# Performance work log

Measured on AMD Instinct MI355X. Metric: run time of the kernel, lower is better.

The kernel has to match this reference:

```python
import jax, jax.numpy as jnp
import numpy as np

N = 100000       # nodes
E = 1600000      # directed edges
D_IN = 64        # input feature dim
D_H = 128        # per-head hidden (num_hidden=256 // 2 heads)
D_OUT = 128      # per-head output (out_dim=256 // 2 heads)
DIR_SEQS = ("OI", "UU")  # per-head direction sequences (already length num_layers=2)
H = len(DIR_SEQS)


def _glorot(key, shape):
    # xavier_uniform with relu gain, matching reset_parameters
    gain = np.sqrt(2.0)
    fan_out, fan_in = shape[-2], shape[-1]
    limit = gain * np.sqrt(6.0 / (fan_in + fan_out))
    return jax.random.uniform(key, shape, jnp.float32, -limit, limit)


def setup_inputs() -> dict:
    key = jax.random.key(0)
    ks = jax.random.split(key, 10)
    x = jax.random.normal(ks[0], (N, D_IN), jnp.float32)
    src = jax.random.randint(ks[1], (E,), 0, N, dtype=jnp.int32)
    dst = jax.random.randint(ks[2], (E,), 0, N, dtype=jnp.int32)
    # stacked per-head params: layer0 (D_IN -> D_H), layer1 (D_H -> D_OUT)
    Wn0 = _glorot(ks[3], (H, D_H, D_IN))
    Ws0 = _glorot(ks[4], (H, D_H, D_IN))
    b0 = jnp.zeros((H, D_H), jnp.float32)
    Wn1 = _glorot(ks[5], (H, D_OUT, D_H))
    Ws1 = _glorot(ks[6], (H, D_OUT, D_H))
    b1 = jnp.zeros((H, D_OUT), jnp.float32)
    return {"x": x, "src": src, "dst": dst,
            "Wn0": Wn0, "Ws0": Ws0, "b0": b0,
            "Wn1": Wn1, "Ws1": Ws1, "b1": b1}


def reference(x, src, dst, Wn0, Ws0, b0, Wn1, Ws1, b1):
    def seg_mean(feat, s, d):
        # DGL mean reduce: zero for nodes with no in-edges
        summ = jax.ops.segment_sum(feat[s], d, num_segments=N)          # [N, F]
        deg = jax.ops.segment_sum(jnp.ones((s.shape[0], 1), feat.dtype), d, num_segments=N)
        return jnp.where(deg > 0, summ / jnp.maximum(deg, 1.0), 0.0)

    def edges_for(c):
        if c == 'O':   # original graph: messages src -> dst
            return src, dst
        if c == 'I':   # reversed graph
            return dst, src
        # 'U': undirected = both directions
        return jnp.concatenate([src, dst]), jnp.concatenate([dst, src])

    def sage_layer(h, s, d, Wn, Ws, b, act):
        in_f, out_f = Wn.shape[1], Wn.shape[0]
        if in_f > out_f:  # lin_before_mp
            h_neigh = seg_mean(h @ Wn.T, s, d)
        else:
            h_neigh = seg_mean(h, s, d) @ Wn.T
        r = h @ Ws.T + b + h_neigh
        return jax.nn.relu(r) if act else r

    outs = []
    for hi, dseq in enumerate(DIR_SEQS):
        h = x
        layers = [(Wn0[hi], Ws0[hi], b0[hi], True),    # hidden layer: relu, no norm
                  (Wn1[hi], Ws1[hi], b1[hi], False)]   # last layer: encoding=False -> no act
        for (Wn, Ws, b, act), c in zip(layers, dseq):
            s, d = edges_for(c)
            h = sage_layer(h, s, d, Wn, Ws, b, act)
        outs.append(h)
    return jnp.concatenate(outs, axis=-1)  # [N, H*D_OUT]
```

## Files before the change

kernel.cpp:

```cpp
#include <hip/hip_runtime.h>
#include <hip/hip_fp8.h>


typedef unsigned short u16;
typedef unsigned int u32;
typedef unsigned char u8;
typedef __bf16 bf16x8 __attribute__((ext_vector_type(8)));
typedef float f32x4 __attribute__((ext_vector_type(4)));

__device__ __forceinline__ u32 f2bf(float f) {
    u32 u = __float_as_uint(f);
    return (u + 0x7fffu + ((u >> 16) & 1u)) >> 16;
}
__device__ __forceinline__ float bf_lo(u32 v) { return __uint_as_float(v << 16); }
__device__ __forceinline__ float bf_hi(u32 v) { return __uint_as_float(v & 0xffff0000u); }
__device__ __forceinline__ u8 f2q(float f) {
    __hip_fp8_e4m3 t(f);
    return *(u8*)&t;
}
__device__ __forceinline__ u32 sprd(u32 v) {
    return __builtin_amdgcn_perm(0u, v, 0x04010400u);
}
__device__ __forceinline__ void acc4(float4& s, u32 v) {
    s.x += __builtin_amdgcn_cvt_f32_fp8(v, 0);
    s.y += __builtin_amdgcn_cvt_f32_fp8(v, 1);
    s.z += __builtin_amdgcn_cvt_f32_fp8(v, 2);
    s.w += __builtin_amdgcn_cvt_f32_fp8(v, 3);
}

__global__ void k_prep(const float* __restrict__ x, u16* __restrict__ xb,
                       u8* __restrict__ xq, int n4, int* __restrict__ cntzero,
                       int* __restrict__ maxzero,
                       const float* __restrict__ Ws0, const float* __restrict__ Wn0,
                       const float* __restrict__ Ws1, const float* __restrict__ Wn1,
                       u16* __restrict__ Wsb0, u16* __restrict__ Wnb0,
                       u16* __restrict__ Wsb1, u16* __restrict__ Wnb1) {
    int i = blockIdx.x * blockDim.x + threadIdx.x;
    if (i < 1024) cntzero[i] = 0;
    if (i < 256) maxzero[i] = 0;
    if (i < n4) {
        float4 v = *(const float4*)&x[(size_t)i * 4];
        u32 p0 = f2bf(v.x) | (f2bf(v.y) << 16);
        u32 p1 = f2bf(v.z) | (f2bf(v.w) << 16);
        *(uint2*)&xb[(size_t)i * 4] = make_uint2(p0, p1);
        u32 q = (u32)f2q(v.x) | ((u32)f2q(v.y) << 8) |
                ((u32)f2q(v.z) << 16) | ((u32)f2q(v.w) << 24);
        *(u32*)&xq[(size_t)i * 4] = q;
        return;
    }
    int t = i - n4;
    if (t < 16384) Wsb0[t] = (u16)f2bf(Ws0[t]);
    else if (t < 32768) Wnb0[t - 16384] = (u16)f2bf(Wn0[t - 16384]);
    else if (t < 65536) Wsb1[t - 32768] = (u16)f2bf(Ws1[t - 32768]);
    else if (t < 98304) Wnb1[t - 65536] = (u16)f2bf(Wn1[t - 65536]);
}


__global__ void __launch_bounds__(256) k_bincnt(
        const int* __restrict__ src, const int* __restrict__ dst,
        int* cntD, int* cntS, int E, int NB) {
    __shared__ int hD[512], hS[512];
    const int tid = threadIdx.x;
    for (int i = tid; i < NB; i += 256) { hD[i] = 0; hS[i] = 0; }
    __syncthreads();
    const int base = (blockIdx.x * 256 + tid) * 8;
#pragma unroll
    for (int i = 0; i < 8; i++) {
        if (base + i < E) {
            atomicAdd(&hD[dst[base + i] >> 8], 1);
            atomicAdd(&hS[src[base + i] >> 8], 1);
        }
    }
    __syncthreads();
    for (int i = tid; i < NB; i += 256) {
        if (hD[i]) atomicAdd(&cntD[i], hD[i]);
        if (hS[i]) atomicAdd(&cntS[i], hS[i]);
    }
}

__global__ void __launch_bounds__(512) k_binscan(
        const int* __restrict__ cntD, const int* __restrict__ cntS,
        int* bbaseD, int* bbaseS, int* curD, int* curS,
        int* off_in, int* off_out, int NB, int N, int E) {
    __shared__ int ts[512];
    const int tid = threadIdx.x;
    int v = (tid < NB) ? cntD[tid] : 0;
    ts[tid] = v;
    __syncthreads();
    for (int ofs = 1; ofs < 512; ofs <<= 1) {
        int t = (tid >= ofs) ? ts[tid - ofs] : 0;
        __syncthreads();
        ts[tid] += t;
        __syncthreads();
    }
    int ex = ts[tid] - v;
    if (tid < NB) { bbaseD[tid] = ex; curD[tid] = ex; }
    if (tid == NB - 1) bbaseD[NB] = ex + v;
    __syncthreads();
    v = (tid < NB) ? cntS[tid] : 0;
    ts[tid] = v;
    __syncthreads();
    for (int ofs = 1; ofs < 512; ofs <<= 1) {
        int t = (tid >= ofs) ? ts[tid - ofs] : 0;
        __syncthreads();
        ts[tid] += t;
        __syncthreads();
    }
    ex = ts[tid] - v;
    if (tid < NB) { bbaseS[tid] = ex; curS[tid] = ex; }
    if (tid == NB - 1) bbaseS[NB] = ex + v;
    if (tid == 0) { off_in[N] = E; off_out[N] = E; }
}

__global__ void __launch_bounds__(256) k_binscatter(
        const int* __restrict__ src, const int* __restrict__ dst,
        int* curD, int* curS, u32* __restrict__ pairsD, u32* __restrict__ pairsS,
        int E, int NB) {
    __shared__ int hD[512], hS[512], bD[512], bS[512];
    const int tid = threadIdx.x;
    for (int i = tid; i < NB; i += 256) { hD[i] = 0; hS[i] = 0; }
    __syncthreads();
    const int base = (blockIdx.x * 256 + tid) * 8;
    int sv[8], dv[8], rD[8], rS[8];
#pragma unroll
    for (int i = 0; i < 8; i++) {
        if (base + i < E) {
            sv[i] = src[base + i];
            dv[i] = dst[base + i];
            rD[i] = atomicAdd(&hD[dv[i] >> 8], 1);
            rS[i] = atomicAdd(&hS[sv[i] >> 8], 1);
        }
    }
    __syncthreads();
    for (int i = tid; i < NB; i += 256) {
        bD[i] = hD[i] ? atomicAdd(&curD[i], hD[i]) : 0;
        bS[i] = hS[i] ? atomicAdd(&curS[i], hS[i]) : 0;
    }
    __syncthreads();
#pragma unroll
    for (int i = 0; i < 8; i++) {
        if (base + i < E) {
            pairsD[bD[dv[i] >> 8] + rD[i]] = ((u32)(dv[i] & 255) << 24) | (u32)sv[i];
            pairsS[bS[sv[i] >> 8] + rS[i]] = ((u32)(sv[i] & 255) << 24) | (u32)dv[i];
        }
    }
}

__global__ void __launch_bounds__(256) k_bucket_csr(
        const u32* __restrict__ pairsD, const u32* __restrict__ pairsS,
        const int* __restrict__ bbaseD, const int* __restrict__ bbaseS,
        int* __restrict__ off_in, int* __restrict__ adj_in,
        int* __restrict__ off_out, int* __restrict__ adj_out, int N) {
    __shared__ int cnt[256], cur[256], ts[256];
    const int b = blockIdx.x >> 1;
    const int arr = blockIdx.x & 1;
    const u32* pairs = arr ? pairsS : pairsD;
    const int* bbase = arr ? bbaseS : bbaseD;
    int* off = arr ? off_out : off_in;
    int* adj = arr ? adj_out : adj_in;
    const int e0 = bbase[b], e1 = bbase[b + 1];
    const int tid = threadIdx.x;
    cnt[tid] = 0;
    __syncthreads();
    for (int e = e0 + tid; e < e1; e += 256) atomicAdd(&cnt[pairs[e] >> 24], 1);
    __syncthreads();
    int v = cnt[tid];
    ts[tid] = v;
    __syncthreads();
    for (int ofs = 1; ofs < 256; ofs <<= 1) {
        int t = (tid >= ofs) ? ts[tid - ofs] : 0;
        __syncthreads();
        ts[tid] += t;
        __syncthreads();
    }
    const int ex = ts[tid] - v;
    const int n = b * 256 + tid;
    if (n < N) off[n] = e0 + ex;
    cur[tid] = e0 + ex;
    __syncthreads();
    for (int e = e0 + tid; e < e1; e += 256) {
        u32 p = pairs[e];
        int w = atomicAdd(&cur[p >> 24], 1);
        adj[w] = (int)(p & 0xFFFFFFu);
    }
}

__global__ void __launch_bounds__(256) k_agg_l0_q(
        const u8* __restrict__ xq,
        const int* __restrict__ off_in, const int* __restrict__ adj_in,
        const int* __restrict__ off_out, const int* __restrict__ adj_out,
        u16* __restrict__ agg0b, u16* __restrict__ aggUb, int n) {
    const int node = blockIdx.x * 4 + (threadIdx.x >> 6);
    const int lane = threadIdx.x & 63;
    if (node >= n) return;
    const int g = lane >> 4;
    const int p = (lane & 15) * 4;
    const int a0 = off_in[node], a1 = off_in[node + 1];
    const int b0 = off_out[node], b1 = off_out[node + 1];
    float4 si = {0.f, 0.f, 0.f, 0.f}, so = {0.f, 0.f, 0.f, 0.f};
    int j = a0;
    for (; j + 15 < a1; j += 16) {
        int i0 = adj_in[j + g], i1 = adj_in[j + 4 + g];
        int i2 = adj_in[j + 8 + g], i3 = adj_in[j + 12 + g];
        u32 v0 = *(const u32*)&xq[(size_t)i0 * 64 + p];
        u32 v1 = *(const u32*)&xq[(size_t)i1 * 64 + p];
        u32 v2 = *(const u32*)&xq[(size_t)i2 * 64 + p];
        u32 v3 = *(const u32*)&xq[(size_t)i3 * 64 + p];
        acc4(si, v0); acc4(si, v1); acc4(si, v2); acc4(si, v3);
    }
    for (; j + 3 < a1; j += 4) {
        int i0 = adj_in[j + g];
        u32 v0 = *(const u32*)&xq[(size_t)i0 * 64 + p];
        acc4(si, v0);
    }
    if (j < a1 && g < a1 - j) {
        int i0 = adj_in[j + g];
        u32 v0 = *(const u32*)&xq[(size_t)i0 * 64 + p];
        acc4(si, v0);
    }
    j = b0;
    for (; j + 15 < b1; j += 16) {
        int i0 = adj_out[j + g], i1 = adj_out[j + 4 + g];
        int i2 = adj_out[j + 8 + g], i3 = adj_out[j + 12 + g];
        u32 v0 = *(const u32*)&xq[(size_t)i0 * 64 + p];
        u32 v1 = *(const u32*)&xq[(size_t)i1 * 64 + p];
        u32 v2 = *(const u32*)&xq[(size_t)i2 * 64 + p];
        u32 v3 = *(const u32*)&xq[(size_t)i3 * 64 + p];
        acc4(so, v0); acc4(so, v1); acc4(so, v2); acc4(so, v3);
    }
    for (; j + 3 < b1; j += 4) {
        int i0 = adj_out[j + g];
        u32 v0 = *(const u32*)&xq[(size_t)i0 * 64 + p];
        acc4(so, v0);
    }
    if (j < b1 && g < b1 - j) {
        int i0 = adj_out[j + g];
        u32 v0 = *(const u32*)&xq[(size_t)i0 * 64 + p];
        acc4(so, v0);
    }
#pragma unroll
    for (int ofs = 16; ofs < 64; ofs <<= 1) {
        si.x += __shfl_xor(si.x, ofs);
        si.y += __shfl_xor(si.y, ofs);
        si.z += __shfl_xor(si.z, ofs);
        si.w += __shfl_xor(si.w, ofs);
        so.x += __shfl_xor(so.x, ofs);
        so.y += __shfl_xor(so.y, ofs);
        so.z += __shfl_xor(so.z, ofs);
        so.w += __shfl_xor(so.w, ofs);
    }
    if (g == 0) {
        const int din = a1 - a0, dout = b1 - b0;
        const int du = din + dout;
        const float fi = din ? 1.f / (float)din : 0.f;
        const float fu = du ? 1.f / (float)du : 0.f;
        uint2 q0, qU;
        q0.x = f2bf(si.x * fi) | (f2bf(si.y * fi) << 16);
        q0.y = f2bf(si.z * fi) | (f2bf(si.w * fi) << 16);
        qU.x = f2bf((si.x + so.x) * fu) | (f2bf((si.y + so.y) * fu) << 16);
        qU.y = f2bf((si.z + so.z) * fu) | (f2bf((si.w + so.w) * fu) << 16);
        *(uint2*)&agg0b[(size_t)node * 64 + p] = q0;
        *(uint2*)&aggUb[(size_t)node * 64 + p] = qU;
    }
}

__global__ void __launch_bounds__(256) k_quant(
        const u16* __restrict__ h1b, const u16* __restrict__ u1b,
        const float* __restrict__ maxH, const float* __restrict__ maxU,
        u8* __restrict__ ob, int N) {
    int i = blockIdx.x * blockDim.x + threadIdx.x;
    const int total = N * 16;
    if (i >= 2 * total) return;
    const int head = (i >= total) ? 1 : 0;
    int t = i - head * total;
    const int row = t >> 4, seg = t & 15;
    const u16* src = head ? u1b : h1b;
    const float* mx = head ? maxU : maxH;
    uint4 v = *(const uint4*)&src[(size_t)row * 128 + seg * 8];
    float4 m0 = *(const float4*)&mx[seg * 8];
    float4 m1 = *(const float4*)&mx[seg * 8 + 4];
    float rs0 = m0.x > 0.f ? 255.f / m0.x : 0.f;
    float rs1 = m0.y > 0.f ? 255.f / m0.y : 0.f;
    float rs2 = m0.z > 0.f ? 255.f / m0.z : 0.f;
    float rs3 = m0.w > 0.f ? 255.f / m0.w : 0.f;
    float rs4 = m1.x > 0.f ? 255.f / m1.x : 0.f;
    float rs5 = m1.y > 0.f ? 255.f / m1.y : 0.f;
    float rs6 = m1.z > 0.f ? 255.f / m1.z : 0.f;
    float rs7 = m1.w > 0.f ? 255.f / m1.w : 0.f;
    u32 q0 = (u32)fminf(rintf(bf_lo(v.x) * rs0), 255.f);
    u32 q1 = (u32)fminf(rintf(bf_hi(v.x) * rs1), 255.f);
    u32 q2 = (u32)fminf(rintf(bf_lo(v.y) * rs2), 255.f);
    u32 q3 = (u32)fminf(rintf(bf_hi(v.y) * rs3), 255.f);
    u32 q4 = (u32)fminf(rintf(bf_lo(v.z) * rs4), 255.f);
    u32 q5 = (u32)fminf(rintf(bf_hi(v.z) * rs5), 255.f);
    u32 q6 = (u32)fminf(rintf(bf_lo(v.w) * rs6), 255.f);
    u32 q7 = (u32)fminf(rintf(bf_hi(v.w) * rs7), 255.f);
    uint2 p;
    p.x = q0 | (q1 << 8) | (q2 << 16) | (q3 << 24);
    p.y = q4 | (q5 << 8) | (q6 << 16) | (q7 << 24);
    *(uint2*)(ob + ((size_t)row << 10) + head * 128 + seg * 8) = p;
}

__global__ void __launch_bounds__(256) k_agg_l1_f(
        const u8* __restrict__ ob,
        const int* __restrict__ off_in, const int* __restrict__ adj_in,
        const int* __restrict__ off_out, const int* __restrict__ adj_out,
        const float* __restrict__ maxH, const float* __restrict__ maxU,
        u16* __restrict__ aggH, int n) {
    const int node = blockIdx.x * 4 + (threadIdx.x >> 6);
    const int lane = threadIdx.x & 63;
    if (node >= n) return;
    const int a0 = off_out[node], a1 = off_out[node + 1];
    const int b0 = off_in[node], b1 = off_in[node + 1];
    u32 sH0 = 0, sH1 = 0, sU0 = 0, sU1 = 0;
    const int lo2 = lane * 2;
    int j = a0;
    for (; j + 7 < a1; j += 8) {
        size_t p0 = ((size_t)adj_out[j] << 10) + lo2;
        size_t p1 = ((size_t)adj_out[j + 1] << 10) + lo2;
        size_t p2 = ((size_t)adj_out[j + 2] << 10) + lo2;
        size_t p3 = ((size_t)adj_out[j + 3] << 10) + lo2;
        size_t p4 = ((size_t)adj_out[j + 4] << 10) + lo2;
        size_t p5 = ((size_t)adj_out[j + 5] << 10) + lo2;
        size_t p6 = ((size_t)adj_out[j + 6] << 10) + lo2;
        size_t p7 = ((size_t)adj_out[j + 7] << 10) + lo2;
        u32 h0 = *(const u16*)(ob + p0), u0 = *(const u16*)(ob + p0 + 128);
        u32 h1 = *(const u16*)(ob + p1), u1 = *(const u16*)(ob + p1 + 128);
        u32 h2 = *(const u16*)(ob + p2), u2 = *(const u16*)(ob + p2 + 128);
        u32 h3 = *(const u16*)(ob + p3), u3 = *(const u16*)(ob + p3 + 128);
        u32 h4 = *(const u16*)(ob + p4), u4 = *(const u16*)(ob + p4 + 128);
        u32 h5 = *(const u16*)(ob + p5), u5 = *(const u16*)(ob + p5 + 128);
        u32 h6 = *(const u16*)(ob + p6), u6 = *(const u16*)(ob + p6 + 128);
        u32 h7 = *(const u16*)(ob + p7), u7 = *(const u16*)(ob + p7 + 128);
        u32 aH = ((sprd(h0) + sprd(h1)) + (sprd(h2) + sprd(h3))) +
                 ((sprd(h4) + sprd(h5)) + (sprd(h6) + sprd(h7)));
        u32 aU = ((sprd(u0) + sprd(u1)) + (sprd(u2) + sprd(u3))) +
                 ((sprd(u4) + sprd(u5)) + (sprd(u6) + sprd(u7)));
        sH0 += aH & 0xFFFFu; sH1 += aH >> 16;
        sU0 += aU & 0xFFFFu; sU1 += aU >> 16;
    }
    for (; j < a1; j++) {
        size_t p = ((size_t)adj_out[j] << 10) + lo2;
        u32 h = *(const u16*)(ob + p), u = *(const u16*)(ob + p + 128);
        sH0 += h & 255; sH1 += h >> 8;
        sU0 += u & 255; sU1 += u >> 8;
    }
    j = b0;
    for (; j + 7 < b1; j += 8) {
        size_t p0 = ((size_t)adj_in[j] << 10) + lo2 + 128;
        size_t p1 = ((size_t)adj_in[j + 1] << 10) + lo2 + 128;
        size_t p2 = ((size_t)adj_in[j + 2] << 10) + lo2 + 128;
        size_t p3 = ((size_t)adj_in[j + 3] << 10) + lo2 + 128;
        size_t p4 = ((size_t)adj_in[j + 4] << 10) + lo2 + 128;
        size_t p5 = ((size_t)adj_in[j + 5] << 10) + lo2 + 128;
        size_t p6 = ((size_t)adj_in[j + 6] << 10) + lo2 + 128;
        size_t p7 = ((size_t)adj_in[j + 7] << 10) + lo2 + 128;
        u32 u0 = *(const u16*)(ob + p0), u1 = *(const u16*)(ob + p1);
        u32 u2 = *(const u16*)(ob + p2), u3 = *(const u16*)(ob + p3);
        u32 u4 = *(const u16*)(ob + p4), u5 = *(const u16*)(ob + p5);
        u32 u6 = *(const u16*)(ob + p6), u7 = *(const u16*)(ob + p7);
        u32 aU = ((sprd(u0) + sprd(u1)) + (sprd(u2) + sprd(u3))) +
                 ((sprd(u4) + sprd(u5)) + (sprd(u6) + sprd(u7)));
        sU0 += aU & 0xFFFFu; sU1 += aU >> 16;
    }
    for (; j < b1; j++) {
        size_t p = ((size_t)adj_in[j] << 10) + lo2 + 128;
        u32 u = *(const u16*)(ob + p);
        sU0 += u & 255; sU1 += u >> 8;
    }
    const int degO = a1 - a0;
    const int degU = degO + (b1 - b0);
    const float invO = degO ? 1.f / (float)degO : 0.f;
    const float invU = degU ? 1.f / (float)degU : 0.f;
    float2 mh = *(const float2*)&maxH[lo2];
    float2 mu = *(const float2*)&maxU[lo2];
    const float c = 1.f / 255.f;
    u32 pH = f2bf((float)sH0 * mh.x * c * invO) |
             (f2bf((float)sH1 * mh.y * c * invO) << 16);
    u32 pU = f2bf((float)sU0 * mu.x * c * invU) |
             (f2bf((float)sU1 * mu.y * c * invU) << 16);
    *(u32*)&aggH[(size_t)node * 128 + lo2] = pH;
    *(u32*)((u8*)ob + ((size_t)node << 10) + 768 + lane * 4) = pU;
}

template <int KC, int OUT_BF16>
__device__ __forceinline__ void gemm_tile(
        const u16* __restrict__ A, int lda,
        const u16* __restrict__ B, int ldb,
        const u16* __restrict__ W1, const u16* __restrict__ W2,
        u8* lds1, u8* lds2, int* lmax,
        const float* __restrict__ bias,
        float* __restrict__ OutF, int ldo, u16* __restrict__ OutB,
        int* __restrict__ colmax, int n, int r0, int nthreads) {
    constexpr int K = KC * 32;
    constexpr int RS = K * 2;
    constexpr int WB = 128 * RS;
    const int tid = threadIdx.x;
    const int lane = tid & 63;

    for (int i = tid * 16; i < WB; i += nthreads * 16) {
        const int row = i / RS;
        const int swz = i ^ ((row & 7) << 4);
        *(uint4*)(lds1 + swz) = *(const uint4*)((const u8*)W1 + i);
        *(uint4*)(lds2 + swz) = *(const uint4*)((const u8*)W2 + i);
    }
    if (OUT_BF16 && tid < 128) lmax[tid] = 0;
    __syncthreads();

    const int arow = r0 + (lane & 15);
    const int crow = (arow < n) ? arow : n - 1;
    const int kof = (lane >> 4) * 8;
    const int kofb = kof * 2;

    bf16x8 a1[KC], a2[KC];
#pragma unroll
    for (int kc = 0; kc < KC; kc++) {
        a1[kc] = *(const bf16x8*)&A[(size_t)crow * lda + kc * 32 + kof];
        a2[kc] = *(const bf16x8*)&B[(size_t)crow * ldb + kc * 32 + kof];
    }
    const int wr = lane & 15;
    const int rbase = r0 + (lane >> 4) * 4;
#pragma unroll
    for (int c = 0; c < 8; c++) {
        f32x4 acc = {0.f, 0.f, 0.f, 0.f};
        const int wrow = c * 16 + wr;
        const int wbase = wrow * RS + kofb;
        const int rsw = (wrow & 7) << 4;
#pragma unroll
        for (int kc = 0; kc < KC; kc++) {
            const int bo = (wbase + kc * 64) ^ rsw;
            acc = __builtin_amdgcn_mfma_f32_16x16x32_bf16(
                a1[kc], *(const bf16x8*)(lds1 + bo), acc, 0, 0, 0);
            acc = __builtin_amdgcn_mfma_f32_16x16x32_bf16(
                a2[kc], *(const bf16x8*)(lds2 + bo), acc, 0, 0, 0);
        }
        const int col = c * 16 + wr;
        const float bv = bias[col];
        float cmax = 0.f;
#pragma unroll
        for (int r = 0; r < 4; r++) {
            const int row = rbase + r;
            if (row < n) {
                float v = acc[r] + bv;
                if (OUT_BF16) {
                    v = fmaxf(v, 0.f);
                    cmax = fmaxf(cmax, v);
                    OutB[(size_t)row * 128 + col] = (u16)f2bf(v);
                } else {
                    __builtin_nontemporal_store(v, &OutF[(size_t)row * ldo + col]);
                }
            }
        }
        if (OUT_BF16) atomicMax(&lmax[col], __float_as_int(cmax));
    }
    if (OUT_BF16) {
        __syncthreads();
        if (tid < 128) atomicMax(&colmax[tid], lmax[tid]);
    }
}

__global__ void __launch_bounds__(512) k_gemm_l0_fused(
        const u16* __restrict__ xb,
        const u16* __restrict__ agg0b, const u16* __restrict__ aggUb,
        const u16* __restrict__ Wsb0, const u16* __restrict__ Wnb0,
        const float* __restrict__ b0,
        u16* __restrict__ h1b, u16* __restrict__ u1b,
        int* __restrict__ maxH, int* __restrict__ maxU, int n, int nblk) {
    __shared__ u8 lds1[128 * 64 * 2], lds2[128 * 64 * 2];
    __shared__ int lmax[128];
    const int head = (blockIdx.x >= nblk) ? 1 : 0;
    const int blk = blockIdx.x - head * nblk;
    const int r0 = blk * 128 + (threadIdx.x >> 6) * 16;
    gemm_tile<2, 1>(xb, 64, head ? aggUb : agg0b, 64,
                    Wsb0 + head * 128 * 64, Wnb0 + head * 128 * 64,
                    lds1, lds2, lmax,
                    b0 + head * 128, (float*)nullptr, 0,
                    head ? u1b : h1b, head ? maxU : maxH, n, r0, 512);
}

__global__ void __launch_bounds__(512) k_gemm_l1_fused(
        const u16* __restrict__ h1b, const u16* __restrict__ u1b,
        const u16* __restrict__ aggH, const u16* __restrict__ aggU,
        const u16* __restrict__ Wsb1, const u16* __restrict__ Wnb1,
        const float* __restrict__ b1,
        float* __restrict__ out, int n, int nblk) {
    __shared__ u8 lds1[128 * 128 * 2], lds2[128 * 128 * 2];
    const int head = (blockIdx.x >= nblk) ? 1 : 0;
    const int blk = blockIdx.x - head * nblk;
    const int r0 = blk * 128 + (threadIdx.x >> 6) * 16;
    if (head == 0) {
        gemm_tile<4, 0>(h1b, 128, aggH, 128, Wsb1, Wnb1, lds1, lds2, (int*)nullptr,
                        b1, out, 256, (u16*)nullptr, (int*)nullptr, n, r0, 512);
    } else {
        gemm_tile<4, 0>(u1b, 128, aggU, 512, Wsb1 + 128 * 128, Wnb1 + 128 * 128,
                        lds1, lds2, (int*)nullptr, b1 + 128, out + 128, 256,
                        (u16*)nullptr, (int*)nullptr, n, r0, 512);
    }
}

extern "C" void kernel_launch(void* const* d_in, const int* in_sizes, int n_in,
                              void* d_out, int out_size, void* d_ws, size_t ws_size,
                              hipStream_t stream) {
    const float* x = (const float*)d_in[0];
    const int* src = (const int*)d_in[1];
    const int* dst = (const int*)d_in[2];
    const float* Wn0 = (const float*)d_in[3];
    const float* Ws0 = (const float*)d_in[4];
    const float* b0 = (const float*)d_in[5];
    const float* Wn1 = (const float*)d_in[6];
    const float* Ws1 = (const float*)d_in[7];
    const float* b1 = (const float*)d_in[8];

    const int N = in_sizes[0] / 64;
    const int E = in_sizes[1];
    float* out = (float*)d_out;
    const int NB = (N + 255) >> 8;

    char* w = (char*)d_ws;
    size_t o = 0;
    auto alloc = [&](size_t bytes) -> void* {
        o = (o + 255) & ~(size_t)255;
        void* p = w + o;
        o += bytes;
        return p;
    };
    int* off_in = (int*)alloc((size_t)(N + 1) * 4);
    int* off_out = (int*)alloc((size_t)(N + 1) * 4);
    int* cntD = (int*)alloc(512 * 4);
    int* cntS = (int*)alloc(512 * 4);
    int* curD = (int*)alloc(512 * 4);
    int* curS = (int*)alloc(512 * 4);
    int* bbaseD = (int*)alloc(513 * 4);
    int* bbaseS = (int*)alloc(513 * 4);
    float* maxH = (float*)alloc(128 * 4);
    float* maxU = (float*)alloc(128 * 4);
    int* adj_in = (int*)alloc((size_t)E * 4);
    int* adj_out = (int*)alloc((size_t)E * 4);
    u16* AGGb = (u16*)alloc((size_t)N * 128 * 2);
    u16* h1b = (u16*)alloc((size_t)N * 128 * 2);
    u16* u1b = (u16*)alloc((size_t)N * 128 * 2);
    u16* Wsb0 = (u16*)alloc(2 * 128 * 64 * 2);
    u16* Wnb0 = (u16*)alloc(2 * 128 * 64 * 2);
    u16* Wsb1 = (u16*)alloc(2 * 128 * 128 * 2);
    u16* Wnb1 = (u16*)alloc(2 * 128 * 128 * 2);
    (void)ws_size;

    u32* pairsD = (u32*)h1b;
    u32* pairsS = (u32*)u1b;
    u16* xb = (u16*)d_out;
    u8* xq = (u8*)d_out + (16 << 20);
    u8* ob = (u8*)d_out;

    const int n4 = N * 64 / 4;
    const int edgeBlocks = ((E + 7) / 8 + 255) / 256;

    k_prep<<<(n4 + 98304 + 255) / 256, 256, 0, stream>>>(
        x, xb, xq, n4, cntD, (int*)maxH, Ws0, Wn0, Ws1, Wn1, Wsb0, Wnb0, Wsb1, Wnb1);

    k_bincnt<<<edgeBlocks, 256, 0, stream>>>(src, dst, cntD, cntS, E, NB);
    k_binscan<<<1, 512, 0, stream>>>(cntD, cntS, bbaseD, bbaseS, curD, curS,
                                     off_in, off_out, NB, N, E);
    k_binscatter<<<edgeBlocks, 256, 0, stream>>>(src, dst, curD, curS, pairsD, pairsS, E, NB);
    k_bucket_csr<<<2 * NB, 256, 0, stream>>>(pairsD, pairsS, bbaseD, bbaseS,
                                             off_in, adj_in, off_out, adj_out, N);

    const int nodeBlocks = (N + 3) / 4;
    const int gemmBlocks128 = (N + 127) / 128;

    u16* agg0b = AGGb;
    u16* aggUb = AGGb + (size_t)N * 64;
    k_agg_l0_q<<<nodeBlocks, 256, 0, stream>>>(xq, off_in, adj_in, off_out, adj_out,
                                               agg0b, aggUb, N);
    k_gemm_l0_fused<<<2 * gemmBlocks128, 512, 0, stream>>>(
        xb, agg0b, aggUb, Wsb0, Wnb0, b0, h1b, u1b, (int*)maxH, (int*)maxU,
        N, gemmBlocks128);

    k_quant<<<(2 * N * 16 + 255) / 256, 256, 0, stream>>>(h1b, u1b, maxH, maxU, ob, N);

    k_agg_l1_f<<<nodeBlocks, 256, 0, stream>>>(ob, off_in, adj_in, off_out, adj_out,
                                               maxH, maxU, AGGb, N);

    k_gemm_l1_fused<<<2 * gemmBlocks128, 512, 0, stream>>>(
        h1b, u1b, AGGb, (const u16*)d_out + 384, Wsb1, Wnb1, b1, out, N, gemmBlocks128);
}
```

Measured before the change: 395.7 us.

## Merge bin counting into prep kernel and widen layer-1 gather loads

Folds the edge bin-count histogram into the prep kernel launch as extra blocks, and replaces the in-kernel zeroing with memset calls. The layer-1 aggregation kernel now splits each wave into two half-waves that each process alternate edges with 4-byte loads instead of 2-byte loads, then combines the halves with a cross-lane shuffle. The aim is fewer kernel launches and fewer, wider gather loads per edge, at the cost of two memset operations, a shuffle reduction, and half the lanes idling during the final write.

```diff
diff --git a/kernel.cpp b/kernel.cpp
--- a/kernel.cpp
+++ b/kernel.cpp
@@ -18,8 +18,11 @@
     __hip_fp8_e4m3 t(f);
     return *(u8*)&t;
 }
-__device__ __forceinline__ u32 sprd(u32 v) {
+__device__ __forceinline__ u32 sprd01(u32 v) {
     return __builtin_amdgcn_perm(0u, v, 0x04010400u);
+}
+__device__ __forceinline__ u32 sprd23(u32 v) {
+    return __builtin_amdgcn_perm(0u, v, 0x04030402u);
 }
 __device__ __forceinline__ void acc4(float4& s, u32 v) {
     s.x += __builtin_amdgcn_cvt_f32_fp8(v, 0);
@@ -28,16 +31,36 @@
     s.w += __builtin_amdgcn_cvt_f32_fp8(v, 3);
 }
 
-__global__ void k_prep(const float* __restrict__ x, u16* __restrict__ xb,
-                       u8* __restrict__ xq, int n4, int* __restrict__ cntzero,
-                       int* __restrict__ maxzero,
-                       const float* __restrict__ Ws0, const float* __restrict__ Wn0,
-                       const float* __restrict__ Ws1, const float* __restrict__ Wn1,
-                       u16* __restrict__ Wsb0, u16* __restrict__ Wnb0,
-                       u16* __restrict__ Wsb1, u16* __restrict__ Wnb1) {
+__global__ void __launch_bounds__(256) k_prep(
+        const float* __restrict__ x, u16* __restrict__ xb,
+        u8* __restrict__ xq, int n4, int prepBlocks,
+        const float* __restrict__ Ws0, const float* __restrict__ Wn0,
+        const float* __restrict__ Ws1, const float* __restrict__ Wn1,
+        u16* __restrict__ Wsb0, u16* __restrict__ Wnb0,
+        u16* __restrict__ Wsb1, u16* __restrict__ Wnb1,
+        const int* __restrict__ src, const int* __restrict__ dst,
+        int* cntD, int* cntS, int E, int NB) {
+    __shared__ int hD[512], hS[512];
+    if (blockIdx.x >= prepBlocks) {
+        const int tid = threadIdx.x;
+        for (int i = tid; i < NB; i += 256) { hD[i] = 0; hS[i] = 0; }
+        __syncthreads();
+        const int base = ((blockIdx.x - prepBlocks) * 256 + tid) * 8;
+#pragma unroll
+        for (int i = 0; i < 8; i++) {
+            if (base + i < E) {
+                atomicAdd(&hD[dst[base + i] >> 8], 1);
+                atomicAdd(&hS[src[base + i] >> 8], 1);
+            }
+        }
+        __syncthreads();
+        for (int i = tid; i < NB; i += 256) {
+            if (hD[i]) atomicAdd(&cntD[i], hD[i]);
+            if (hS[i]) atomicAdd(&cntS[i], hS[i]);
+        }
+        return;
+    }
     int i = blockIdx.x * blockDim.x + threadIdx.x;
-    if (i < 1024) cntzero[i] = 0;
-    if (i < 256) maxzero[i] = 0;
     if (i < n4) {
         float4 v = *(const float4*)&x[(size_t)i * 4];
         u32 p0 = f2bf(v.x) | (f2bf(v.y) << 16);
@@ -55,28 +78,6 @@
     else if (t < 98304) Wnb1[t - 65536] = (u16)f2bf(Wn1[t - 65536]);
 }
 
-
-__global__ void __launch_bounds__(256) k_bincnt(
-        const int* __restrict__ src, const int* __restrict__ dst,
-        int* cntD, int* cntS, int E, int NB) {
-    __shared__ int hD[512], hS[512];
-    const int tid = threadIdx.x;
-    for (int i = tid; i < NB; i += 256) { hD[i] = 0; hS[i] = 0; }
-    __syncthreads();
-    const int base = (blockIdx.x * 256 + tid) * 8;
-#pragma unroll
-    for (int i = 0; i < 8; i++) {
-        if (base + i < E) {
-            atomicAdd(&hD[dst[base + i] >> 8], 1);
-            atomicAdd(&hS[src[base + i] >> 8], 1);
-        }
-    }
-    __syncthreads();
-    for (int i = tid; i < NB; i += 256) {
-        if (hD[i]) atomicAdd(&cntD[i], hD[i]);
-        if (hS[i]) atomicAdd(&cntS[i], hS[i]);
-    }
-}
 
 __global__ void __launch_bounds__(512) k_binscan(
         const int* __restrict__ cntD, const int* __restrict__ cntS,
@@ -310,77 +311,81 @@
     const int node = blockIdx.x * 4 + (threadIdx.x >> 6);
     const int lane = threadIdx.x & 63;
     if (node >= n) return;
+    const int h = lane >> 5;
+    const int q = lane & 31;
+    const int qb = q * 4;
     const int a0 = off_out[node], a1 = off_out[node + 1];
     const int b0 = off_in[node], b1 = off_in[node + 1];
-    u32 sH0 = 0, sH1 = 0, sU0 = 0, sU1 = 0;
-    const int lo2 = lane * 2;
-    int j = a0;
-    for (; j + 7 < a1; j += 8) {
-        size_t p0 = ((size_t)adj_out[j] << 10) + lo2;
-        size_t p1 = ((size_t)adj_out[j + 1] << 10) + lo2;
-        size_t p2 = ((size_t)adj_out[j + 2] << 10) + lo2;
-        size_t p3 = ((size_t)adj_out[j + 3] << 10) + lo2;
-        size_t p4 = ((size_t)adj_out[j + 4] << 10) + lo2;
-        size_t p5 = ((size_t)adj_out[j + 5] << 10) + lo2;
-        size_t p6 = ((size_t)adj_out[j + 6] << 10) + lo2;
-        size_t p7 = ((size_t)adj_out[j + 7] << 10) + lo2;
-        u32 h0 = *(const u16*)(ob + p0), u0 = *(const u16*)(ob + p0 + 128);
-        u32 h1 = *(const u16*)(ob + p1), u1 = *(const u16*)(ob + p1 + 128);
-        u32 h2 = *(const u16*)(ob + p2), u2 = *(const u16*)(ob + p2 + 128);
-        u32 h3 = *(const u16*)(ob + p3), u3 = *(const u16*)(ob + p3 + 128);
-        u32 h4 = *(const u16*)(ob + p4), u4 = *(const u16*)(ob + p4 + 128);
-        u32 h5 = *(const u16*)(ob + p5), u5 = *(const u16*)(ob + p5 + 128);
-        u32 h6 = *(const u16*)(ob + p6), u6 = *(const u16*)(ob + p6 + 128);
-        u32 h7 = *(const u16*)(ob + p7), u7 = *(const u16*)(ob + p7 + 128);
-        u32 aH = ((sprd(h0) + sprd(h1)) + (sprd(h2) + sprd(h3))) +
-                 ((sprd(h4) + sprd(h5)) + (sprd(h6) + sprd(h7)));
-        u32 aU = ((sprd(u0) + sprd(u1)) + (sprd(u2) + sprd(u3))) +
-                 ((sprd(u4) + sprd(u5)) + (sprd(u6) + sprd(u7)));
-        sH0 += aH & 0xFFFFu; sH1 += aH >> 16;
-        sU0 += aU & 0xFFFFu; sU1 += aU >> 16;
-    }
-    for (; j < a1; j++) {
-        size_t p = ((size_t)adj_out[j] << 10) + lo2;
-        u32 h = *(const u16*)(ob + p), u = *(const u16*)(ob + p + 128);
-        sH0 += h & 255; sH1 += h >> 8;
-        sU0 += u & 255; sU1 += u >> 8;
-    }
-    j = b0;
-    for (; j + 7 < b1; j += 8) {
-        size_t p0 = ((size_t)adj_in[j] << 10) + lo2 + 128;
-        size_t p1 = ((size_t)adj_in[j + 1] << 10) + lo2 + 128;
-        size_t p2 = ((size_t)adj_in[j + 2] << 10) + lo2 + 128;
-        size_t p3 = ((size_t)adj_in[j + 3] << 10) + lo2 + 128;
-        size_t p4 = ((size_t)adj_in[j + 4] << 10) + lo2 + 128;
-        size_t p5 = ((size_t)adj_in[j + 5] << 10) + lo2 + 128;
-        size_t p6 = ((size_t)adj_in[j + 6] << 10) + lo2 + 128;
-        size_t p7 = ((size_t)adj_in[j + 7] << 10) + lo2 + 128;
-        u32 u0 = *(const u16*)(ob + p0), u1 = *(const u16*)(ob + p1);
-        u32 u2 = *(const u16*)(ob + p2), u3 = *(const u16*)(ob + p3);
-        u32 u4 = *(const u16*)(ob + p4), u5 = *(const u16*)(ob + p5);
-        u32 u6 = *(const u16*)(ob + p6), u7 = *(const u16*)(ob + p7);
-        u32 aU = ((sprd(u0) + sprd(u1)) + (sprd(u2) + sprd(u3))) +
-                 ((sprd(u4) + sprd(u5)) + (sprd(u6) + sprd(u7)));
-        sU0 += aU & 0xFFFFu; sU1 += aU >> 16;
-    }
-    for (; j < b1; j++) {
-        size_t p = ((size_t)adj_in[j] << 10) + lo2 + 128;
-        u32 u = *(const u16*)(ob + p);
-        sU0 += u & 255; sU1 += u >> 8;
-    }
-    const int degO = a1 - a0;
-    const int degU = degO + (b1 - b0);
-    const float invO = degO ? 1.f / (float)degO : 0.f;
-    const float invU = degU ? 1.f / (float)degU : 0.f;
-    float2 mh = *(const float2*)&maxH[lo2];
-    float2 mu = *(const float2*)&maxU[lo2];
-    const float c = 1.f / 255.f;
-    u32 pH = f2bf((float)sH0 * mh.x * c * invO) |
-             (f2bf((float)sH1 * mh.y * c * invO) << 16);
-    u32 pU = f2bf((float)sU0 * mu.x * c * invU) |
-             (f2bf((float)sU1 * mu.y * c * invU) << 16);
-    *(u32*)&aggH[(size_t)node * 128 + lo2] = pH;
-    *(u32*)((u8*)ob + ((size_t)node << 10) + 768 + lane * 4) = pU;
+    u32 SH0 = 0, SH1 = 0, SH2 = 0, SH3 = 0;
+    u32 SU0 = 0, SU1 = 0, SU2 = 0, SU3 = 0;
+    for (int base = a0; base < a1; base += 256) {
+        const int end = (a1 - base < 256) ? a1 : base + 256;
+        u32 tHa = 0, tHb = 0, tUa = 0, tUb = 0;
+        int j = base;
+        for (; j + 1 < end; j += 2) {
+            size_t p = ((size_t)adj_out[j + h] << 10) + qb;
+            u32 hv = *(const u32*)(ob + p);
+            u32 uv = *(const u32*)(ob + p + 128);
+            tHa += sprd01(hv); tHb += sprd23(hv);
+            tUa += sprd01(uv); tUb += sprd23(uv);
+        }
+        if (j < end && h == 0) {
+            size_t p = ((size_t)adj_out[j] << 10) + qb;
+            u32 hv = *(const u32*)(ob + p);
+            u32 uv = *(const u32*)(ob + p + 128);
+            tHa += sprd01(hv); tHb += sprd23(hv);
+            tUa += sprd01(uv); tUb += sprd23(uv);
+        }
+        SH0 += tHa & 0xFFFFu; SH1 += tHa >> 16;
+        SH2 += tHb & 0xFFFFu; SH3 += tHb >> 16;
+        SU0 += tUa & 0xFFFFu; SU1 += tUa >> 16;
+        SU2 += tUb & 0xFFFFu; SU3 += tUb >> 16;
+    }
+    for (int base = b0; base < b1; base += 256) {
+        const int end = (b1 - base < 256) ? b1 : base + 256;
+        u32 tUa = 0, tUb = 0;
+        int j = base;
+        for (; j + 1 < end; j += 2) {
+            size_t p = ((size_t)adj_in[j + h] << 10) + qb + 128;
+            u32 uv = *(const u32*)(ob + p);
+            tUa += sprd01(uv); tUb += sprd23(uv);
+        }
+        if (j < end && h == 0) {
+            size_t p = ((size_t)adj_in[j] << 10) + qb + 128;
+            u32 uv = *(const u32*)(ob + p);
+            tUa += sprd01(uv); tUb += sprd23(uv);
+        }
+        SU0 += tUa & 0xFFFFu; SU1 += tUa >> 16;
+        SU2 += tUb & 0xFFFFu; SU3 += tUb >> 16;
+    }
+    SH0 += (u32)__shfl_xor((int)SH0, 32);
+    SH1 += (u32)__shfl_xor((int)SH1, 32);
+    SH2 += (u32)__shfl_xor((int)SH2, 32);
+    SH3 += (u32)__shfl_xor((int)SH3, 32);
+    SU0 += (u32)__shfl_xor((int)SU0, 32);
+    SU1 += (u32)__shfl_xor((int)SU1, 32);
+    SU2 += (u32)__shfl_xor((int)SU2, 32);
+    SU3 += (u32)__shfl_xor((int)SU3, 32);
+    if (lane < 32) {
+        const int degO = a1 - a0;
+        const int degU = degO + (b1 - b0);
+        const float invO = degO ? 1.f / (float)degO : 0.f;
+        const float invU = degU ? 1.f / (float)degU : 0.f;
+        float4 mh = *(const float4*)&maxH[qb];
+        float4 mu = *(const float4*)&maxU[qb];
+        const float c = 1.f / 255.f;
+        uint2 pH, pU;
+        pH.x = f2bf((float)SH0 * mh.x * c * invO) |
+               (f2bf((float)SH1 * mh.y * c * invO) << 16);
+        pH.y = f2bf((float)SH2 * mh.z * c * invO) |
+               (f2bf((float)SH3 * mh.w * c * invO) << 16);
+        pU.x = f2bf((float)SU0 * mu.x * c * invU) |
+               (f2bf((float)SU1 * mu.y * c * invU) << 16);
+        pU.y = f2bf((float)SU2 * mu.z * c * invU) |
+               (f2bf((float)SU3 * mu.w * c * invU) << 16);
+        *(uint2*)&aggH[(size_t)node * 128 + qb] = pH;
+        *(uint2*)((u8*)ob + ((size_t)node << 10) + 768 + qb * 2) = pU;
+    }
 }
 
 template <int KC, int OUT_BF16>
@@ -553,11 +558,15 @@
 
     const int n4 = N * 64 / 4;
     const int edgeBlocks = ((E + 7) / 8 + 255) / 256;
-
-    k_prep<<<(n4 + 98304 + 255) / 256, 256, 0, stream>>>(
-        x, xb, xq, n4, cntD, (int*)maxH, Ws0, Wn0, Ws1, Wn1, Wsb0, Wnb0, Wsb1, Wnb1);
-
-    k_bincnt<<<edgeBlocks, 256, 0, stream>>>(src, dst, cntD, cntS, E, NB);
+    const int prepBlocks = (n4 + 98304 + 255) / 256;
+
+    hipMemsetAsync(cntD, 0, 2 * 512 * 4, stream);
+    hipMemsetAsync(maxH, 0, 2 * 128 * 4, stream);
+
+    k_prep<<<prepBlocks + edgeBlocks, 256, 0, stream>>>(
+        x, xb, xq, n4, prepBlocks, Ws0, Wn0, Ws1, Wn1,
+        Wsb0, Wnb0, Wsb1, Wnb1, src, dst, cntD, cntS, E, NB);
+
     k_binscan<<<1, 512, 0, stream>>>(cntD, cntS, bbaseD, bbaseS, curD, curS,
                                      off_in, off_out, NB, N, E);
     k_binscatter<<<edgeBlocks, 256, 0, stream>>>(src, dst, curD, curS, pairsD, pairsS, E, NB);
```

New measurement: 459.5 us. +16.1%, slower.
